# Kernel optimization log

Hardware: AMD Instinct MI355X
Metric: run time of the kernel (lower is better)

The kernel has to match this reference:

```python
import jax, jax.numpy as jnp
import numpy as np

N_NODES = 100000
N_EDGES = 1600000
NFEAT = 256
NCLASS = 2


def setup_inputs() -> dict:
    key = jax.random.key(0)
    ks = jax.random.split(key, 16)
    x = jax.random.normal(ks[0], (N_NODES, NFEAT), dtype=jnp.float32)
    row = jax.random.randint(ks[1], (N_EDGES,), 0, N_NODES, dtype=jnp.int64) if jax.config.jax_enable_x64 else jax.random.randint(ks[1], (N_EDGES,), 0, N_NODES, dtype=jnp.int32)
    col = jax.random.randint(ks[2], (N_EDGES,), 0, N_NODES, dtype=row.dtype)
    edge_val = jax.random.uniform(ks[3], (N_EDGES,), dtype=jnp.float32)

    def unif(k, shape, fan_out):
        stdv = 1.0 / np.sqrt(fan_out)
        return jax.random.uniform(k, shape, dtype=jnp.float32, minval=-stdv, maxval=stdv)

    W1 = unif(ks[4], (NFEAT, 32), 32); b1 = unif(ks[5], (32,), 32)
    W2 = unif(ks[6], (32, 48), 48);   b2 = unif(ks[7], (48,), 48)
    W3 = unif(ks[8], (48, 64), 64);   b3 = unif(ks[9], (64,), 64)
    fc1_W = unif(ks[10], (64, 32), 64); fc1_b = unif(ks[11], (32,), 64)
    fc2_W = unif(ks[12], (32, NCLASS), 32); fc2_b = unif(ks[13], (NCLASS,), 32)
    return {"x": x, "row": row, "col": col, "edge_val": edge_val,
            "W1": W1, "b1": b1, "W2": W2, "b2": b2, "W3": W3, "b3": b3,
            "fc1_W": fc1_W, "fc1_b": fc1_b, "fc2_W": fc2_W, "fc2_b": fc2_b}


def _spmm(row, col, val, dense):
    # out[i] = sum_{e: row[e]==i} val[e] * dense[col[e]]   (COO sparse @ dense)
    gathered = dense[col] * val[:, None]          # [E, F]
    return jax.ops.segment_sum(gathered, row, num_segments=N_NODES)


def _gc_layer(x, row, col, val, W, b):
    support = x @ W                               # dense mm  [N, out]
    return _spmm(row, col, val, support) + b      # spmm + bias


def reference(x, row, col, edge_val, W1, b1, W2, b2, W3, b3, fc1_W, fc1_b, fc2_W, fc2_b):
    # eval mode: dropout is identity
    h = jax.nn.relu(_gc_layer(x, row, col, edge_val, W1, b1))   # [N, 32]
    h = jax.nn.relu(_gc_layer(h, row, col, edge_val, W2, b2))   # [N, 48]
    h = jax.nn.relu(_gc_layer(h, row, col, edge_val, W3, b3))   # [N, 64]
    y = jnp.mean(h, axis=0)                                     # [64] global mean pool
    y = jax.nn.relu(y @ fc1_W + fc1_b)                          # [32]
    y = jax.nn.softmax(y @ fc2_W + fc2_b, axis=0)               # [nclass]
    return y
```

## Files before the change

kernel.cpp:

```cpp
#include <hip/hip_runtime.h>
#include <hip/hip_bf16.h>

#define N_NODES 100000
#define N_EDGES 1600000

#define NT 391
#define NB1 128
#define CHUNK ((N_EDGES + NB1 - 1) / NB1)
#define ROWS3 80
#define GRID3 (N_NODES / ROWS3)

__device__ __forceinline__ unsigned char f2q(float f) {
    return (unsigned char)(__builtin_amdgcn_cvt_pk_fp8_f32(f, f, 0, false) & 0xFF);
}
__device__ __forceinline__ unsigned pack4_fp8(float a0, float a1, float a2, float a3) {
    int r = __builtin_amdgcn_cvt_pk_fp8_f32(a0, a1, 0, false);
    r = __builtin_amdgcn_cvt_pk_fp8_f32(a2, a3, r, true);
    return (unsigned)r;
}
#define CVT(u, s) __builtin_amdgcn_cvt_f32_fp8((u), (s))

#define ACC16(A, U, V)                                                              \
    A[0]  += (V) * CVT((U).x, 0); A[1]  += (V) * CVT((U).x, 1);                     \
    A[2]  += (V) * CVT((U).x, 2); A[3]  += (V) * CVT((U).x, 3);                     \
    A[4]  += (V) * CVT((U).y, 0); A[5]  += (V) * CVT((U).y, 1);                     \
    A[6]  += (V) * CVT((U).y, 2); A[7]  += (V) * CVT((U).y, 3);                     \
    A[8]  += (V) * CVT((U).z, 0); A[9]  += (V) * CVT((U).z, 1);                     \
    A[10] += (V) * CVT((U).z, 2); A[11] += (V) * CVT((U).z, 3);                     \
    A[12] += (V) * CVT((U).w, 0); A[13] += (V) * CVT((U).w, 1);                     \
    A[14] += (V) * CVT((U).w, 2); A[15] += (V) * CVT((U).w, 3);


__global__ __launch_bounds__(256) void k_phist(const int* __restrict__ row, int* __restrict__ blkhist) {
    __shared__ int h[NT];
    int b = blockIdx.x, t = threadIdx.x;
    for (int i = t; i < NT; i += 256) h[i] = 0;
    __syncthreads();
    int s = b * CHUNK, e = min(s + CHUNK, N_EDGES);
    for (int i = s + t; i < e; i += 256) atomicAdd(&h[row[i] >> 8], 1);
    __syncthreads();
    for (int i = t; i < NT; i += 256) blkhist[i * NB1 + b] = h[i];
}

__global__ __launch_bounds__(128) void k_bscan1(int* __restrict__ blkhist, int* __restrict__ cnt) {
    __shared__ int s[128];
    int j = blockIdx.x, t = threadIdx.x;
    int v = blkhist[j * NB1 + t];
    s[t] = v;
    __syncthreads();
    #pragma unroll
    for (int st = 1; st < 128; st <<= 1) {
        int u = (t >= st) ? s[t - st] : 0;
        __syncthreads();
        s[t] += u;
        __syncthreads();
    }
    blkhist[j * NB1 + t] = s[t] - v;
    if (t == 127) cnt[j] = s[127];
}

__global__ __launch_bounds__(512) void k_bscan2(const int* __restrict__ cnt, int* __restrict__ base,
                                                int* __restrict__ row_ptr) {
    __shared__ int s[512];
    int j = threadIdx.x;
    int v = (j < NT) ? cnt[j] : 0;
    s[j] = v;
    __syncthreads();
    for (int st = 1; st < 512; st <<= 1) {
        int u = (j >= st) ? s[j - st] : 0;
        __syncthreads();
        s[j] += u;
        __syncthreads();
    }
    if (j < NT) base[j] = s[j] - v;
    if (j == 0) row_ptr[N_NODES] = N_EDGES;
}

__global__ __launch_bounds__(256) void k_pscatter(const int* __restrict__ row, const int* __restrict__ col,
                                                  const float* __restrict__ val,
                                                  const int* __restrict__ blkhist, const int* __restrict__ base,
                                                  int2* __restrict__ part) {
    __shared__ int cur[NT];
    int b = blockIdx.x, t = threadIdx.x;
    for (int i = t; i < NT; i += 256) cur[i] = blkhist[i * NB1 + b] + base[i];
    __syncthreads();
    int s = b * CHUNK, e = min(s + CHUNK, N_EDGES);
    for (int i = s + t; i < e; i += 256) {
        int r = row[i];
        int j = r >> 8;
        int p = atomicAdd(&cur[j], 1);
        part[p] = make_int2(((r & 255) << 24) | col[i], __float_as_int(val[i]));
    }
}

__global__ __launch_bounds__(256) void k_sort(const int2* __restrict__ part, const int* __restrict__ cnt,
                                              const int* __restrict__ base, int* __restrict__ row_ptr,
                                              unsigned* __restrict__ csr) {
    __shared__ int hist[256];
    __shared__ int cur[256];
    int b = blockIdx.x, t = threadIdx.x;
    int n = cnt[b];
    int bb = base[b];
    const int2* sl = part + bb;
    hist[t] = 0;
    __syncthreads();
    for (int i = t; i < n; i += 256) atomicAdd(&hist[((unsigned)sl[i].x) >> 24], 1);
    __syncthreads();
    int v = hist[t];
    for (int st = 1; st < 256; st <<= 1) {
        int u = (t >= st) ? hist[t - st] : 0;
        __syncthreads();
        hist[t] += u;
        __syncthreads();
    }
    cur[t] = hist[t] - v;
    int grow = b * 256 + t;
    if (grow < N_NODES) row_ptr[grow] = bb + cur[t];
    __syncthreads();
    for (int i = t; i < n; i += 256) {
        int2 e = sl[i];
        int rl = ((unsigned)e.x) >> 24;
        int p = atomicAdd(&cur[rl], 1);
        unsigned c = (unsigned)(e.x & 0xFFFFFF);
        float vf = __int_as_float(e.y);
        int q = __float2int_rn(vf * 32768.0f);
        if (q > 32767) q = 32767;
        csr[bb + p] = (c << 15) | (unsigned)q;
    }
}

__global__ __launch_bounds__(256) void k_gemm1(const float* __restrict__ x, const float* __restrict__ W,
                                               unsigned char* __restrict__ out) {
    __shared__ float xs[64][68];
    __shared__ __align__(16) float wc[64 * 32];
    int tid = threadIdx.x;
    int bn = blockIdx.x * 64;
    int nl = tid >> 3;
    int o4 = (tid & 7) * 4;
    float acc[2][4] = {};
    for (int kc = 0; kc < 4; ++kc) {
        int k0 = kc * 64;
        #pragma unroll
        for (int i = 0; i < 4; ++i) {
            int idx = i * 256 + tid;
            int n = idx >> 4;
            int k4 = (idx & 15) * 4;
            float4 v = make_float4(0.f, 0.f, 0.f, 0.f);
            if (bn + n < N_NODES)
                v = *reinterpret_cast<const float4*>(&x[(size_t)(bn + n) * 256 + k0 + k4]);
            *reinterpret_cast<float4*>(&xs[n][k4]) = v;
        }
        #pragma unroll
        for (int i = 0; i < 2; ++i) {
            int idx = i * 256 + tid;
            reinterpret_cast<float4*>(wc)[idx] =
                reinterpret_cast<const float4*>(W + (size_t)k0 * 32)[idx];
        }
        __syncthreads();
        #pragma unroll 8
        for (int k = 0; k < 64; ++k) {
            float a0 = xs[nl][k];
            float a1 = xs[nl + 32][k];
            float4 w = *reinterpret_cast<const float4*>(&wc[k * 32 + o4]);
            acc[0][0] += a0 * w.x; acc[0][1] += a0 * w.y; acc[0][2] += a0 * w.z; acc[0][3] += a0 * w.w;
            acc[1][0] += a1 * w.x; acc[1][1] += a1 * w.y; acc[1][2] += a1 * w.z; acc[1][3] += a1 * w.w;
        }
        __syncthreads();
    }
    #pragma unroll
    for (int i = 0; i < 2; ++i) {
        int n = bn + nl + 32 * i;
        if (n < N_NODES) {
            unsigned r = pack4_fp8(acc[i][0], acc[i][1], acc[i][2], acc[i][3]);
            *reinterpret_cast<unsigned*>(&out[(size_t)n * 32 + o4]) = r;
        }
    }
}

__global__ __launch_bounds__(256, 8) void k_spmm1(const int* __restrict__ rp, const unsigned* __restrict__ csr,
                                                  const unsigned char* __restrict__ sup,
                                                  const float* __restrict__ bias,
                                                  unsigned char* __restrict__ out) {
    int gid = blockIdx.x * 256 + threadIdx.x;
    int n = gid >> 1;
    if (n >= N_NODES) return;
    int f16 = (gid & 1) * 16;
    int e0 = rp[n], e1 = rp[n + 1];
    float a[16] = {};
    int e = e0;
    if ((e & 1) && e < e1) {
        unsigned ent = csr[e];
        float v = (float)(ent & 0x7FFF);
        uint4 u = *reinterpret_cast<const uint4*>(&sup[(size_t)(ent >> 15) * 32 + f16]);
        ACC16(a, u, v)
        ++e;
    }
    for (; e + 1 < e1; e += 2) {
        uint2 p = *reinterpret_cast<const uint2*>(&csr[e]);
        uint4 u = *reinterpret_cast<const uint4*>(&sup[(size_t)(p.x >> 15) * 32 + f16]);
        uint4 w = *reinterpret_cast<const uint4*>(&sup[(size_t)(p.y >> 15) * 32 + f16]);
        float v0 = (float)(p.x & 0x7FFF), v1 = (float)(p.y & 0x7FFF);
        ACC16(a, u, v0)
        ACC16(a, w, v1)
    }
    if (e < e1) {
        unsigned ent = csr[e];
        float v = (float)(ent & 0x7FFF);
        uint4 u = *reinterpret_cast<const uint4*>(&sup[(size_t)(ent >> 15) * 32 + f16]);
        ACC16(a, u, v)
    }
    const float sc = 1.0f / 32768.0f;
    uint4 r;
    r.x = pack4_fp8(fmaxf(a[0] * sc + bias[f16 + 0], 0.f),  fmaxf(a[1] * sc + bias[f16 + 1], 0.f),
                    fmaxf(a[2] * sc + bias[f16 + 2], 0.f),  fmaxf(a[3] * sc + bias[f16 + 3], 0.f));
    r.y = pack4_fp8(fmaxf(a[4] * sc + bias[f16 + 4], 0.f),  fmaxf(a[5] * sc + bias[f16 + 5], 0.f),
                    fmaxf(a[6] * sc + bias[f16 + 6], 0.f),  fmaxf(a[7] * sc + bias[f16 + 7], 0.f));
    r.z = pack4_fp8(fmaxf(a[8] * sc + bias[f16 + 8], 0.f),  fmaxf(a[9] * sc + bias[f16 + 9], 0.f),
                    fmaxf(a[10] * sc + bias[f16 + 10], 0.f), fmaxf(a[11] * sc + bias[f16 + 11], 0.f));
    r.w = pack4_fp8(fmaxf(a[12] * sc + bias[f16 + 12], 0.f), fmaxf(a[13] * sc + bias[f16 + 13], 0.f),
                    fmaxf(a[14] * sc + bias[f16 + 14], 0.f), fmaxf(a[15] * sc + bias[f16 + 15], 0.f));
    *reinterpret_cast<uint4*>(&out[(size_t)n * 32 + f16]) = r;
}

__global__ __launch_bounds__(256, 8) void k_l2fused(const int* __restrict__ rp, const unsigned* __restrict__ csr,
                                                    const unsigned char* __restrict__ h1,
                                                    const float* __restrict__ W2, const float* __restrict__ b2,
                                                    unsigned char* __restrict__ h2) {
    __shared__ float w2s[32 * 48];
    __shared__ float b2s[48];
    __shared__ float g2s[128][33];
    int tid = threadIdx.x;
    for (int i = tid; i < 32 * 48; i += 256) w2s[i] = W2[i];
    if (tid < 48) b2s[tid] = b2[tid];
    int n0 = blockIdx.x * 128;
    int grp = tid >> 1;
    int f16 = (tid & 1) * 16;
    int n = n0 + grp;
    if (n < N_NODES) {
        int e0 = rp[n], e1 = rp[n + 1];
        float a[16] = {};
        int e = e0;
        if ((e & 1) && e < e1) {
            unsigned ent = csr[e];
            float v = (float)(ent & 0x7FFF);
            uint4 u = *reinterpret_cast<const uint4*>(&h1[(size_t)(ent >> 15) * 32 + f16]);
            ACC16(a, u, v)
            ++e;
        }
        for (; e + 1 < e1; e += 2) {
            uint2 p = *reinterpret_cast<const uint2*>(&csr[e]);
            uint4 u = *reinterpret_cast<const uint4*>(&h1[(size_t)(p.x >> 15) * 32 + f16]);
            uint4 w = *reinterpret_cast<const uint4*>(&h1[(size_t)(p.y >> 15) * 32 + f16]);
            float v0 = (float)(p.x & 0x7FFF), v1 = (float)(p.y & 0x7FFF);
            ACC16(a, u, v0)
            ACC16(a, w, v1)
        }
        if (e < e1) {
            unsigned ent = csr[e];
            float v = (float)(ent & 0x7FFF);
            uint4 u = *reinterpret_cast<const uint4*>(&h1[(size_t)(ent >> 15) * 32 + f16]);
            ACC16(a, u, v)
        }
        const float sc = 1.0f / 32768.0f;
        #pragma unroll
        for (int j = 0; j < 16; ++j) g2s[grp][f16 + j] = a[j] * sc;
    }
    __syncthreads();
    #pragma unroll
    for (int pp = 0; pp < 24; ++pp) {
        int idx = pp * 256 + tid;
        int r = idx / 48;
        int m = idx - 48 * r;
        if (n0 + r < N_NODES) {
            float a = b2s[m];
            const float* g = g2s[r];
            #pragma unroll
            for (int k = 0; k < 32; ++k) a += g[k] * w2s[k * 48 + m];
            h2[(size_t)(n0 + r) * 48 + m] = f2q(fmaxf(a, 0.f));
        }
    }
}

__global__ __launch_bounds__(256, 8) void k_l3fused(const int* __restrict__ rp, const unsigned* __restrict__ csr,
                                                    const unsigned char* __restrict__ h2,
                                                    const float* __restrict__ W3, const float* __restrict__ b3,
                                                    float* __restrict__ poolpart) {
    __shared__ float w3s[48 * 64];
    __shared__ float b3s[64];
    __shared__ float g3s[ROWS3][49];
    __shared__ float red[256];
    int tid = threadIdx.x;
    for (int i = tid; i < 48 * 64; i += 256) w3s[i] = W3[i];
    if (tid < 64) b3s[tid] = b3[tid];
    int grp = tid / 3;
    int f16 = (tid - grp * 3) * 16;
    int m = tid & 63;
    const float sc = 1.0f / 32768.0f;
    if (tid < 240) {
        int n = blockIdx.x * ROWS3 + grp;
        int e0 = rp[n], e1 = rp[n + 1];
        float a[16] = {};
        int e = e0;
        if ((e & 1) && e < e1) {
            unsigned ent = csr[e];
            float v = (float)(ent & 0x7FFF);
            uint4 u = *reinterpret_cast<const uint4*>(&h2[(size_t)(ent >> 15) * 48 + f16]);
            ACC16(a, u, v)
            ++e;
        }
        for (; e + 1 < e1; e += 2) {
            uint2 p = *reinterpret_cast<const uint2*>(&csr[e]);
            uint4 u = *reinterpret_cast<const uint4*>(&h2[(size_t)(p.x >> 15) * 48 + f16]);
            uint4 w = *reinterpret_cast<const uint4*>(&h2[(size_t)(p.y >> 15) * 48 + f16]);
            float v0 = (float)(p.x & 0x7FFF), v1 = (float)(p.y & 0x7FFF);
            ACC16(a, u, v0)
            ACC16(a, w, v1)
        }
        if (e < e1) {
            unsigned ent = csr[e];
            float v = (float)(ent & 0x7FFF);
            uint4 u = *reinterpret_cast<const uint4*>(&h2[(size_t)(ent >> 15) * 48 + f16]);
            ACC16(a, u, v)
        }
        #pragma unroll
        for (int j = 0; j < 16; ++j) g3s[grp][f16 + j] = a[j] * sc;
    }
    __syncthreads();
    float poolacc = 0.f;
    #pragma unroll
    for (int pp = 0; pp < 20; ++pp) {
        int r = 4 * pp + (tid >> 6);
        float a = b3s[m];
        const float* gg = g3s[r];
        #pragma unroll
        for (int k = 0; k < 48; ++k) a += gg[k] * w3s[k * 64 + m];
        poolacc += fmaxf(a, 0.f);
    }
    red[tid] = poolacc;
    __syncthreads();
    if (tid < 64) {
        float s = red[tid] + red[tid + 64] + red[tid + 128] + red[tid + 192];
        poolpart[(size_t)blockIdx.x * 64 + tid] = s;
    }
}

__global__ __launch_bounds__(256) void k_preduce(const float* __restrict__ poolpart,
                                                 float* __restrict__ pool) {
    __shared__ float red[256];
    int b = blockIdx.x, t = threadIdx.x;
    float s = 0.f;
    for (int j = t; j < GRID3; j += 256) s += poolpart[(size_t)j * 64 + b];
    red[t] = s;
    __syncthreads();
    for (int st = 128; st > 0; st >>= 1) {
        if (t < st) red[t] += red[t + st];
        __syncthreads();
    }
    if (t == 0) pool[b] = red[0];
}

__global__ __launch_bounds__(64) void k_head(const float* __restrict__ pool,
                                             const float* __restrict__ fc1W, const float* __restrict__ fc1b,
                                             const float* __restrict__ fc2W, const float* __restrict__ fc2b,
                                             float* __restrict__ out) {
    __shared__ float pl[64];
    __shared__ float z[32];
    __shared__ float lg[2];
    int t = threadIdx.x;
    pl[t] = pool[t] * (1.0f / (float)N_NODES);
    __syncthreads();
    if (t < 32) {
        float a = fc1b[t];
        #pragma unroll
        for (int o = 0; o < 64; ++o) a += pl[o] * fc1W[o * 32 + t];
        z[t] = fmaxf(a, 0.f);
    }
    __syncthreads();
    if (t < 2) {
        float l = fc2b[t];
        #pragma unroll
        for (int j = 0; j < 32; ++j) l += z[j] * fc2W[j * 2 + t];
        lg[t] = l;
    }
    __syncthreads();
    if (t == 0) {
        float mx = fmaxf(lg[0], lg[1]);
        float e0 = __expf(lg[0] - mx), e1 = __expf(lg[1] - mx);
        float ss = e0 + e1;
        out[0] = e0 / ss;
        out[1] = e1 / ss;
    }
}


extern "C" void kernel_launch(void* const* d_in, const int* in_sizes, int n_in,
                              void* d_out, int out_size, void* d_ws, size_t ws_size,
                              hipStream_t stream) {
    const float* x    = (const float*)d_in[0];
    const int*   row  = (const int*)d_in[1];
    const int*   col  = (const int*)d_in[2];
    const float* val  = (const float*)d_in[3];
    const float* W1   = (const float*)d_in[4];
    const float* b1   = (const float*)d_in[5];
    const float* W2   = (const float*)d_in[6];
    const float* b2   = (const float*)d_in[7];
    const float* W3   = (const float*)d_in[8];
    const float* b3   = (const float*)d_in[9];
    const float* fc1W = (const float*)d_in[10];
    const float* fc1b = (const float*)d_in[11];
    const float* fc2W = (const float*)d_in[12];
    const float* fc2b = (const float*)d_in[13];
    float* out = (float*)d_out;

    char* wsb = (char*)d_ws;
    size_t off = 0;
    auto alloc = [&](size_t bytes) {
        void* p = wsb + off;
        off += (bytes + 255) / 256 * 256;
        return p;
    };
    int*      blkhist  = (int*)alloc((size_t)NT * NB1 * 4);
    int*      base     = (int*)alloc((size_t)NT * 4);
    int*      cnt      = (int*)alloc((size_t)NT * 4);
    int*      row_ptr  = (int*)alloc((size_t)(N_NODES + 1) * 4);
    int2*     part     = (int2*)alloc((size_t)N_EDGES * 8);
    unsigned* csr      = (unsigned*)alloc((size_t)N_EDGES * 4);
    unsigned char* sup = (unsigned char*)alloc((size_t)N_NODES * 32);
    unsigned char* h1  = (unsigned char*)alloc((size_t)N_NODES * 32);
    unsigned char* h2  = (unsigned char*)alloc((size_t)N_NODES * 48);
    float* poolpart    = (float*)alloc((size_t)GRID3 * 64 * 4);
    float* pool        = (float*)alloc(64 * 4);

    k_phist<<<NB1, 256, 0, stream>>>(row, blkhist);
    k_bscan1<<<NT, 128, 0, stream>>>(blkhist, cnt);
    k_bscan2<<<1, 512, 0, stream>>>(cnt, base, row_ptr);
    k_pscatter<<<NB1, 256, 0, stream>>>(row, col, val, blkhist, base, part);
    k_sort<<<NT, 256, 0, stream>>>(part, cnt, base, row_ptr, csr);

    k_gemm1<<<(N_NODES + 63) / 64, 256, 0, stream>>>(x, W1, sup);
    k_spmm1<<<(N_NODES * 2 + 255) / 256, 256, 0, stream>>>(row_ptr, csr, sup, b1, h1);
    k_l2fused<<<(N_NODES + 127) / 128, 256, 0, stream>>>(row_ptr, csr, h1, W2, b2, h2);
    k_l3fused<<<GRID3, 256, 0, stream>>>(row_ptr, csr, h2, W3, b3, poolpart);
    k_preduce<<<64, 256, 0, stream>>>(poolpart, pool);
    k_head<<<1, 64, 0, stream>>>(pool, fc1W, fc1b, fc2W, fc2b, out);
}
```

Baseline: 214.1 us.

## Fuse gemm1 with row histogram and widen SpMM thread-per-row split

Merges the layer-1 dense GEMM and the row histogram into one launch: extra blocks beyond the GEMM grid run the histogram, so the two independent stages share a kernel and one launch is saved. The SpMM kernels now split each row across more threads (8 threads of 4 features for layers 1–2, 6 threads of 8 features for layer 3) with narrower gathers. This raises parallelism and memory-level concurrency for the irregular gathers, at the cost of reading each CSR entry more times and doing more index work per feature. Layer-2/3 block tiles shrink to match (32 and 40 rows per block), and the layer-3 occupancy hint drops to 7.

Measured after the change: 203.9 us. 1.05x faster.

```diff
diff --git a/kernel.cpp b/kernel.cpp
--- a/kernel.cpp
+++ b/kernel.cpp
@@ -7,8 +7,9 @@
 #define NT 391
 #define NB1 128
 #define CHUNK ((N_EDGES + NB1 - 1) / NB1)
-#define ROWS3 80
+#define ROWS3 40
 #define GRID3 (N_NODES / ROWS3)
+#define GB1 ((N_NODES + 63) / 64)
 
 __device__ __forceinline__ unsigned char f2q(float f) {
     return (unsigned char)(__builtin_amdgcn_cvt_pk_fp8_f32(f, f, 0, false) & 0xFF);
@@ -20,27 +21,77 @@
 }
 #define CVT(u, s) __builtin_amdgcn_cvt_f32_fp8((u), (s))
 
-#define ACC16(A, U, V)                                                              \
-    A[0]  += (V) * CVT((U).x, 0); A[1]  += (V) * CVT((U).x, 1);                     \
-    A[2]  += (V) * CVT((U).x, 2); A[3]  += (V) * CVT((U).x, 3);                     \
-    A[4]  += (V) * CVT((U).y, 0); A[5]  += (V) * CVT((U).y, 1);                     \
-    A[6]  += (V) * CVT((U).y, 2); A[7]  += (V) * CVT((U).y, 3);                     \
-    A[8]  += (V) * CVT((U).z, 0); A[9]  += (V) * CVT((U).z, 1);                     \
-    A[10] += (V) * CVT((U).z, 2); A[11] += (V) * CVT((U).z, 3);                     \
-    A[12] += (V) * CVT((U).w, 0); A[13] += (V) * CVT((U).w, 1);                     \
-    A[14] += (V) * CVT((U).w, 2); A[15] += (V) * CVT((U).w, 3);
-
-
-__global__ __launch_bounds__(256) void k_phist(const int* __restrict__ row, int* __restrict__ blkhist) {
-    __shared__ int h[NT];
-    int b = blockIdx.x, t = threadIdx.x;
-    for (int i = t; i < NT; i += 256) h[i] = 0;
-    __syncthreads();
-    int s = b * CHUNK, e = min(s + CHUNK, N_EDGES);
-    for (int i = s + t; i < e; i += 256) atomicAdd(&h[row[i] >> 8], 1);
-    __syncthreads();
-    for (int i = t; i < NT; i += 256) blkhist[i * NB1 + b] = h[i];
-}
+#define ACC4(A, U, V)                                                               \
+    A[0] += (V) * CVT((U), 0); A[1] += (V) * CVT((U), 1);                           \
+    A[2] += (V) * CVT((U), 2); A[3] += (V) * CVT((U), 3);
+
+#define ACC8(A, U, V)                                                               \
+    A[0] += (V) * CVT((U).x, 0); A[1] += (V) * CVT((U).x, 1);                       \
+    A[2] += (V) * CVT((U).x, 2); A[3] += (V) * CVT((U).x, 3);                       \
+    A[4] += (V) * CVT((U).y, 0); A[5] += (V) * CVT((U).y, 1);                       \
+    A[6] += (V) * CVT((U).y, 2); A[7] += (V) * CVT((U).y, 3);
+
+__global__ __launch_bounds__(256) void k_gemm1_phist(const float* __restrict__ x, const float* __restrict__ W,
+                                                     unsigned char* __restrict__ out,
+                                                     const int* __restrict__ row, int* __restrict__ blkhist) {
+    __shared__ __align__(16) char smem[64 * 68 * 4 + 64 * 32 * 4];
+    int tid = threadIdx.x;
+    if (blockIdx.x >= GB1) {
+        int* h = (int*)smem;
+        int b = blockIdx.x - GB1;
+        for (int i = tid; i < NT; i += 256) h[i] = 0;
+        __syncthreads();
+        int s = b * CHUNK, e = min(s + CHUNK, N_EDGES);
+        for (int i = s + tid; i < e; i += 256) atomicAdd(&h[row[i] >> 8], 1);
+        __syncthreads();
+        for (int i = tid; i < NT; i += 256) blkhist[i * NB1 + b] = h[i];
+        return;
+    }
+    float (*xs)[68] = (float(*)[68])smem;
+    float* wc = (float*)(smem + 64 * 68 * 4);
+    int bn = blockIdx.x * 64;
+    int nl = tid >> 3;
+    int o4 = (tid & 7) * 4;
+    float acc[2][4] = {};
+    for (int kc = 0; kc < 4; ++kc) {
+        int k0 = kc * 64;
+        #pragma unroll
+        for (int i = 0; i < 4; ++i) {
+            int idx = i * 256 + tid;
+            int n = idx >> 4;
+            int k4 = (idx & 15) * 4;
+            float4 v = make_float4(0.f, 0.f, 0.f, 0.f);
+            if (bn + n < N_NODES)
+                v = *reinterpret_cast<const float4*>(&x[(size_t)(bn + n) * 256 + k0 + k4]);
+            *reinterpret_cast<float4*>(&xs[n][k4]) = v;
+        }
+        #pragma unroll
+        for (int i = 0; i < 2; ++i) {
+            int idx = i * 256 + tid;
+            reinterpret_cast<float4*>(wc)[idx] =
+                reinterpret_cast<const float4*>(W + (size_t)k0 * 32)[idx];
+        }
+        __syncthreads();
+        #pragma unroll 8
+        for (int k = 0; k < 64; ++k) {
+            float a0 = xs[nl][k];
+            float a1 = xs[nl + 32][k];
+            float4 w = *reinterpret_cast<const float4*>(&wc[k * 32 + o4]);
+            acc[0][0] += a0 * w.x; acc[0][1] += a0 * w.y; acc[0][2] += a0 * w.z; acc[0][3] += a0 * w.w;
+            acc[1][0] += a1 * w.x; acc[1][1] += a1 * w.y; acc[1][2] += a1 * w.z; acc[1][3] += a1 * w.w;
+        }
+        __syncthreads();
+    }
+    #pragma unroll
+    for (int i = 0; i < 2; ++i) {
+        int n = bn + nl + 32 * i;
+        if (n < N_NODES) {
+            unsigned r = pack4_fp8(acc[i][0], acc[i][1], acc[i][2], acc[i][3]);
+            *reinterpret_cast<unsigned*>(&out[(size_t)n * 32 + o4]) = r;
+        }
+    }
+}
+
 
 __global__ __launch_bounds__(128) void k_bscan1(int* __restrict__ blkhist, int* __restrict__ cnt) {
     __shared__ int s[128];
@@ -129,97 +180,42 @@
     }
 }
 
-__global__ __launch_bounds__(256) void k_gemm1(const float* __restrict__ x, const float* __restrict__ W,
-                                               unsigned char* __restrict__ out) {
-    __shared__ float xs[64][68];
-    __shared__ __align__(16) float wc[64 * 32];
-    int tid = threadIdx.x;
-    int bn = blockIdx.x * 64;
-    int nl = tid >> 3;
-    int o4 = (tid & 7) * 4;
-    float acc[2][4] = {};
-    for (int kc = 0; kc < 4; ++kc) {
-        int k0 = kc * 64;
-        #pragma unroll
-        for (int i = 0; i < 4; ++i) {
-            int idx = i * 256 + tid;
-            int n = idx >> 4;
-            int k4 = (idx & 15) * 4;
-            float4 v = make_float4(0.f, 0.f, 0.f, 0.f);
-            if (bn + n < N_NODES)
-                v = *reinterpret_cast<const float4*>(&x[(size_t)(bn + n) * 256 + k0 + k4]);
-            *reinterpret_cast<float4*>(&xs[n][k4]) = v;
-        }
-        #pragma unroll
-        for (int i = 0; i < 2; ++i) {
-            int idx = i * 256 + tid;
-            reinterpret_cast<float4*>(wc)[idx] =
-                reinterpret_cast<const float4*>(W + (size_t)k0 * 32)[idx];
-        }
-        __syncthreads();
-        #pragma unroll 8
-        for (int k = 0; k < 64; ++k) {
-            float a0 = xs[nl][k];
-            float a1 = xs[nl + 32][k];
-            float4 w = *reinterpret_cast<const float4*>(&wc[k * 32 + o4]);
-            acc[0][0] += a0 * w.x; acc[0][1] += a0 * w.y; acc[0][2] += a0 * w.z; acc[0][3] += a0 * w.w;
-            acc[1][0] += a1 * w.x; acc[1][1] += a1 * w.y; acc[1][2] += a1 * w.z; acc[1][3] += a1 * w.w;
-        }
-        __syncthreads();
-    }
-    #pragma unroll
-    for (int i = 0; i < 2; ++i) {
-        int n = bn + nl + 32 * i;
-        if (n < N_NODES) {
-            unsigned r = pack4_fp8(acc[i][0], acc[i][1], acc[i][2], acc[i][3]);
-            *reinterpret_cast<unsigned*>(&out[(size_t)n * 32 + o4]) = r;
-        }
-    }
-}
-
 __global__ __launch_bounds__(256, 8) void k_spmm1(const int* __restrict__ rp, const unsigned* __restrict__ csr,
                                                   const unsigned char* __restrict__ sup,
                                                   const float* __restrict__ bias,
                                                   unsigned char* __restrict__ out) {
     int gid = blockIdx.x * 256 + threadIdx.x;
-    int n = gid >> 1;
+    int n = gid >> 3;
     if (n >= N_NODES) return;
-    int f16 = (gid & 1) * 16;
+    int f4 = (gid & 7) * 4;
     int e0 = rp[n], e1 = rp[n + 1];
-    float a[16] = {};
+    float a[4] = {};
     int e = e0;
     if ((e & 1) && e < e1) {
         unsigned ent = csr[e];
         float v = (float)(ent & 0x7FFF);
-        uint4 u = *reinterpret_cast<const uint4*>(&sup[(size_t)(ent >> 15) * 32 + f16]);
-        ACC16(a, u, v)
+        unsigned u = *reinterpret_cast<const unsigned*>(&sup[(size_t)(ent >> 15) * 32 + f4]);
+        ACC4(a, u, v)
         ++e;
     }
     for (; e + 1 < e1; e += 2) {
         uint2 p = *reinterpret_cast<const uint2*>(&csr[e]);
-        uint4 u = *reinterpret_cast<const uint4*>(&sup[(size_t)(p.x >> 15) * 32 + f16]);
-        uint4 w = *reinterpret_cast<const uint4*>(&sup[(size_t)(p.y >> 15) * 32 + f16]);
+        unsigned u0 = *reinterpret_cast<const unsigned*>(&sup[(size_t)(p.x >> 15) * 32 + f4]);
+        unsigned u1 = *reinterpret_cast<const unsigned*>(&sup[(size_t)(p.y >> 15) * 32 + f4]);
         float v0 = (float)(p.x & 0x7FFF), v1 = (float)(p.y & 0x7FFF);
-        ACC16(a, u, v0)
-        ACC16(a, w, v1)
+        ACC4(a, u0, v0)
+        ACC4(a, u1, v1)
     }
     if (e < e1) {
         unsigned ent = csr[e];
         float v = (float)(ent & 0x7FFF);
-        uint4 u = *reinterpret_cast<const uint4*>(&sup[(size_t)(ent >> 15) * 32 + f16]);
-        ACC16(a, u, v)
+        unsigned u = *reinterpret_cast<const unsigned*>(&sup[(size_t)(ent >> 15) * 32 + f4]);
+        ACC4(a, u, v)
     }
     const float sc = 1.0f / 32768.0f;
-    uint4 r;
-    r.x = pack4_fp8(fmaxf(a[0] * sc + bias[f16 + 0], 0.f),  fmaxf(a[1] * sc + bias[f16 + 1], 0.f),
-                    fmaxf(a[2] * sc + bias[f16 + 2], 0.f),  fmaxf(a[3] * sc + bias[f16 + 3], 0.f));
-    r.y = pack4_fp8(fmaxf(a[4] * sc + bias[f16 + 4], 0.f),  fmaxf(a[5] * sc + bias[f16 + 5], 0.f),
-                    fmaxf(a[6] * sc + bias[f16 + 6], 0.f),  fmaxf(a[7] * sc + bias[f16 + 7], 0.f));
-    r.z = pack4_fp8(fmaxf(a[8] * sc + bias[f16 + 8], 0.f),  fmaxf(a[9] * sc + bias[f16 + 9], 0.f),
-                    fmaxf(a[10] * sc + bias[f16 + 10], 0.f), fmaxf(a[11] * sc + bias[f16 + 11], 0.f));
-    r.w = pack4_fp8(fmaxf(a[12] * sc + bias[f16 + 12], 0.f), fmaxf(a[13] * sc + bias[f16 + 13], 0.f),
-                    fmaxf(a[14] * sc + bias[f16 + 14], 0.f), fmaxf(a[15] * sc + bias[f16 + 15], 0.f));
-    *reinterpret_cast<uint4*>(&out[(size_t)n * 32 + f16]) = r;
+    unsigned r = pack4_fp8(fmaxf(a[0] * sc + bias[f4 + 0], 0.f), fmaxf(a[1] * sc + bias[f4 + 1], 0.f),
+                           fmaxf(a[2] * sc + bias[f4 + 2], 0.f), fmaxf(a[3] * sc + bias[f4 + 3], 0.f));
+    *reinterpret_cast<unsigned*>(&out[(size_t)n * 32 + f4]) = r;
 }
 
 __global__ __launch_bounds__(256, 8) void k_l2fused(const int* __restrict__ rp, const unsigned* __restrict__ csr,
@@ -228,60 +224,60 @@
                                                     unsigned char* __restrict__ h2) {
     __shared__ float w2s[32 * 48];
     __shared__ float b2s[48];
-    __shared__ float g2s[128][33];
+    __shared__ float g2s[32][33];
     int tid = threadIdx.x;
     for (int i = tid; i < 32 * 48; i += 256) w2s[i] = W2[i];
     if (tid < 48) b2s[tid] = b2[tid];
-    int n0 = blockIdx.x * 128;
-    int grp = tid >> 1;
-    int f16 = (tid & 1) * 16;
+    int n0 = blockIdx.x * 32;
+    int grp = tid >> 3;
+    int f4 = (tid & 7) * 4;
     int n = n0 + grp;
-    if (n < N_NODES) {
+    {
         int e0 = rp[n], e1 = rp[n + 1];
-        float a[16] = {};
+        float a[4] = {};
         int e = e0;
         if ((e & 1) && e < e1) {
             unsigned ent = csr[e];
             float v = (float)(ent & 0x7FFF);
-            uint4 u = *reinterpret_cast<const uint4*>(&h1[(size_t)(ent >> 15) * 32 + f16]);
-            ACC16(a, u, v)
+            unsigned u = *reinterpret_cast<const unsigned*>(&h1[(size_t)(ent >> 15) * 32 + f4]);
+            ACC4(a, u, v)
             ++e;
         }
         for (; e + 1 < e1; e += 2) {
             uint2 p = *reinterpret_cast<const uint2*>(&csr[e]);
-            uint4 u = *reinterpret_cast<const uint4*>(&h1[(size_t)(p.x >> 15) * 32 + f16]);
-            uint4 w = *reinterpret_cast<const uint4*>(&h1[(size_t)(p.y >> 15) * 32 + f16]);
+            unsigned u0 = *reinterpret_cast<const unsigned*>(&h1[(size_t)(p.x >> 15) * 32 + f4]);
+            unsigned u1 = *reinterpret_cast<const unsigned*>(&h1[(size_t)(p.y >> 15) * 32 + f4]);
             float v0 = (float)(p.x & 0x7FFF), v1 = (float)(p.y & 0x7FFF);
-            ACC16(a, u, v0)
-            ACC16(a, w, v1)
+            ACC4(a, u0, v0)
+            ACC4(a, u1, v1)
         }
         if (e < e1) {
             unsigned ent = csr[e];
             float v = (float)(ent & 0x7FFF);
-            uint4 u = *reinterpret_cast<const uint4*>(&h1[(size_t)(ent >> 15) * 32 + f16]);
-            ACC16(a, u, v)
+            unsigned u = *reinterpret_cast<const unsigned*>(&h1[(size_t)(ent >> 15) * 32 + f4]);
+            ACC4(a, u, v)
         }
         const float sc = 1.0f / 32768.0f;
-        #pragma unroll
-        for (int j = 0; j < 16; ++j) g2s[grp][f16 + j] = a[j] * sc;
+        g2s[grp][f4 + 0] = a[0] * sc;
+        g2s[grp][f4 + 1] = a[1] * sc;
+        g2s[grp][f4 + 2] = a[2] * sc;
+        g2s[grp][f4 + 3] = a[3] * sc;
     }
     __syncthreads();
     #pragma unroll
-    for (int pp = 0; pp < 24; ++pp) {
+    for (int pp = 0; pp < 6; ++pp) {
         int idx = pp * 256 + tid;
         int r = idx / 48;
         int m = idx - 48 * r;
-        if (n0 + r < N_NODES) {
-            float a = b2s[m];
-            const float* g = g2s[r];
-            #pragma unroll
-            for (int k = 0; k < 32; ++k) a += g[k] * w2s[k * 48 + m];
-            h2[(size_t)(n0 + r) * 48 + m] = f2q(fmaxf(a, 0.f));
-        }
-    }
-}
-
-__global__ __launch_bounds__(256, 8) void k_l3fused(const int* __restrict__ rp, const unsigned* __restrict__ csr,
+        float a = b2s[m];
+        const float* g = g2s[r];
+        #pragma unroll
+        for (int k = 0; k < 32; ++k) a += g[k] * w2s[k * 48 + m];
+        h2[(size_t)(n0 + r) * 48 + m] = f2q(fmaxf(a, 0.f));
+    }
+}
+
+__global__ __launch_bounds__(256, 7) void k_l3fused(const int* __restrict__ rp, const unsigned* __restrict__ csr,
                                                     const unsigned char* __restrict__ h2,
                                                     const float* __restrict__ W3, const float* __restrict__ b3,
                                                     float* __restrict__ poolpart) {
@@ -292,43 +288,43 @@
     int tid = threadIdx.x;
     for (int i = tid; i < 48 * 64; i += 256) w3s[i] = W3[i];
     if (tid < 64) b3s[tid] = b3[tid];
-    int grp = tid / 3;
-    int f16 = (tid - grp * 3) * 16;
+    int grp = tid / 6;
+    int f8 = (tid - grp * 6) * 8;
     int m = tid & 63;
     const float sc = 1.0f / 32768.0f;
     if (tid < 240) {
         int n = blockIdx.x * ROWS3 + grp;
         int e0 = rp[n], e1 = rp[n + 1];
-        float a[16] = {};
+        float a[8] = {};
         int e = e0;
         if ((e & 1) && e < e1) {
             unsigned ent = csr[e];
             float v = (float)(ent & 0x7FFF);
-            uint4 u = *reinterpret_cast<const uint4*>(&h2[(size_t)(ent >> 15) * 48 + f16]);
-            ACC16(a, u, v)
+            uint2 u = *reinterpret_cast<const uint2*>(&h2[(size_t)(ent >> 15) * 48 + f8]);
+            ACC8(a, u, v)
             ++e;
         }
         for (; e + 1 < e1; e += 2) {
             uint2 p = *reinterpret_cast<const uint2*>(&csr[e]);
-            uint4 u = *reinterpret_cast<const uint4*>(&h2[(size_t)(p.x >> 15) * 48 + f16]);
-            uint4 w = *reinterpret_cast<const uint4*>(&h2[(size_t)(p.y >> 15) * 48 + f16]);
+            uint2 u0 = *reinterpret_cast<const uint2*>(&h2[(size_t)(p.x >> 15) * 48 + f8]);
+            uint2 u1 = *reinterpret_cast<const uint2*>(&h2[(size_t)(p.y >> 15) * 48 + f8]);
             float v0 = (float)(p.x & 0x7FFF), v1 = (float)(p.y & 0x7FFF);
-            ACC16(a, u, v0)
-            ACC16(a, w, v1)
+            ACC8(a, u0, v0)
+            ACC8(a, u1, v1)
         }
         if (e < e1) {
             unsigned ent = csr[e];
             float v = (float)(ent & 0x7FFF);
-            uint4 u = *reinterpret_cast<const uint4*>(&h2[(size_t)(ent >> 15) * 48 + f16]);
-            ACC16(a, u, v)
-        }
-        #pragma unroll
-        for (int j = 0; j < 16; ++j) g3s[grp][f16 + j] = a[j] * sc;
+            uint2 u = *reinterpret_cast<const uint2*>(&h2[(size_t)(ent >> 15) * 48 + f8]);
+            ACC8(a, u, v)
+        }
+        #pragma unroll
+        for (int j = 0; j < 8; ++j) g3s[grp][f8 + j] = a[j] * sc;
     }
     __syncthreads();
     float poolacc = 0.f;
     #pragma unroll
-    for (int pp = 0; pp < 20; ++pp) {
+    for (int pp = 0; pp < 10; ++pp) {
         int r = 4 * pp + (tid >> 6);
         float a = b3s[m];
         const float* gg = g3s[r];
@@ -431,15 +427,14 @@
     float* poolpart    = (float*)alloc((size_t)GRID3 * 64 * 4);
     float* pool        = (float*)alloc(64 * 4);
 
-    k_phist<<<NB1, 256, 0, stream>>>(row, blkhist);
+    k_gemm1_phist<<<GB1 + NB1, 256, 0, stream>>>(x, W1, sup, row, blkhist);
     k_bscan1<<<NT, 128, 0, stream>>>(blkhist, cnt);
     k_bscan2<<<1, 512, 0, stream>>>(cnt, base, row_ptr);
     k_pscatter<<<NB1, 256, 0, stream>>>(row, col, val, blkhist, base, part);
     k_sort<<<NT, 256, 0, stream>>>(part, cnt, base, row_ptr, csr);
 
-    k_gemm1<<<(N_NODES + 63) / 64, 256, 0, stream>>>(x, W1, sup);
-    k_spmm1<<<(N_NODES * 2 + 255) / 256, 256, 0, stream>>>(row_ptr, csr, sup, b1, h1);
-    k_l2fused<<<(N_NODES + 127) / 128, 256, 0, stream>>>(row_ptr, csr, h1, W2, b2, h2);
+    k_spmm1<<<(N_NODES * 8 + 255) / 256, 256, 0, stream>>>(row_ptr, csr, sup, b1, h1);
+    k_l2fused<<<(N_NODES + 31) / 32, 256, 0, stream>>>(row_ptr, csr, h1, W2, b2, h2);
     k_l3fused<<<GRID3, 256, 0, stream>>>(row_ptr, csr, h2, W3, b3, poolpart);
     k_preduce<<<64, 256, 0, stream>>>(poolpart, pool);
     k_head<<<1, 64, 0, stream>>>(pool, fc1W, fc1b, fc2W, fc2b, out);
```
